# Performance work log

Measured on AMD Instinct MI355X. Metric: run time of the kernel, lower is better.

The kernel has to match this reference:

```python
import jax, jax.numpy as jnp
import numpy as np

N_BITS = 4096
CHANNELS = 48
WIDTH = 1024
HEIGHT = 1024


def setup_inputs() -> dict:
    key = jax.random.key(0)
    bits = jax.random.normal(key, (N_BITS,), dtype=jnp.float32)
    return {"bits": bits}


def reference(bits):
    # map_range = width*height // 8 * 8; with 1024x1024 this is exactly width*height
    map_range = (WIDTH * HEIGHT) // 8 * 8
    idx = jnp.arange(map_range) % N_BITS            # bit index for each pixel (row-major, x=i//W, y=i%W)
    vals = jnp.where(jnp.abs(bits[idx]) > 0.5, 1.0, 0.0).astype(jnp.float32)
    rows = map_range // WIDTH                        # == HEIGHT here (square map, fully covered)
    grid = jnp.zeros((WIDTH, HEIGHT), dtype=jnp.float32)
    grid = grid.at[:rows, :].set(vals.reshape(rows, WIDTH))
    # every channel gets an identical copy
    out = jnp.broadcast_to(grid[None, :, :], (CHANNELS, WIDTH, HEIGHT))
    return jnp.asarray(out)
```

## Files before the change

kernel.cpp:

```cpp
#include <hip/hip_runtime.h>


#define N4       12582912u
#define NBLK     2048u
#define NTHR     (NBLK * 256u)
#define NITER    (N4 / NTHR)

__global__ __launch_bounds__(256) void
LinearTextEmbedding_57604101374655_kernel(const float4* __restrict__ bits4,
                                          float4* __restrict__ out) {
    unsigned t = blockIdx.x * 256u + threadIdx.x;
    float4 b = bits4[t & 1023u];
    float4 v;
    v.x = (fabsf(b.x) > 0.5f) ? 1.0f : 0.0f;
    v.y = (fabsf(b.y) > 0.5f) ? 1.0f : 0.0f;
    v.z = (fabsf(b.z) > 0.5f) ? 1.0f : 0.0f;
    v.w = (fabsf(b.w) > 0.5f) ? 1.0f : 0.0f;
    float4* p = out + t;
#pragma unroll
    for (unsigned i = 0; i < NITER; ++i) {
        *p = v;
        p += NTHR;
    }
}

extern "C" void kernel_launch(void* const* d_in, const int* in_sizes, int n_in,
                              void* d_out, int out_size, void* d_ws, size_t ws_size,
                              hipStream_t stream) {
    const float4* bits4 = (const float4*)d_in[0];
    float4* out = (float4*)d_out;
    LinearTextEmbedding_57604101374655_kernel<<<NBLK, 256, 0, stream>>>(bits4, out);
}
```

Baseline: 195.8 us.

## Use many small blocks writing contiguous chunks with nontemporal stores

Replaces the persistent grid-stride loop (2048 blocks, 24 stores each) with 12288 blocks that each write one contiguous 16 KB chunk using four nontemporal vector stores. Each thread loads and binarizes four bit vectors. The aim is to cut cache pollution on the 201 MB write-only output and to improve write streaming. The cost is more block launches and redundant input loads per block.

```diff
diff --git a/kernel.cpp b/kernel.cpp
--- a/kernel.cpp
+++ b/kernel.cpp
@@ -1,33 +1,40 @@
 #include <hip/hip_runtime.h>
 
 
-#define N4       12582912u
-#define NBLK     2048u
-#define NTHR     (NBLK * 256u)
-#define NITER    (N4 / NTHR)
+typedef float v4f __attribute__((ext_vector_type(4)));
 
-__global__ __launch_bounds__(256) void
-LinearTextEmbedding_57604101374655_kernel(const float4* __restrict__ bits4,
-                                          float4* __restrict__ out) {
-    unsigned t = blockIdx.x * 256u + threadIdx.x;
-    float4 b = bits4[t & 1023u];
-    float4 v;
+#define N4    12582912u
+#define BLK4  1024u
+#define NBLK  (N4 / BLK4)
+
+__device__ __forceinline__ v4f bin4(v4f b) {
+    v4f v;
     v.x = (fabsf(b.x) > 0.5f) ? 1.0f : 0.0f;
     v.y = (fabsf(b.y) > 0.5f) ? 1.0f : 0.0f;
     v.z = (fabsf(b.z) > 0.5f) ? 1.0f : 0.0f;
     v.w = (fabsf(b.w) > 0.5f) ? 1.0f : 0.0f;
-    float4* p = out + t;
-#pragma unroll
-    for (unsigned i = 0; i < NITER; ++i) {
-        *p = v;
-        p += NTHR;
-    }
+    return v;
+}
+
+__global__ __launch_bounds__(256) void
+LinearTextEmbedding_57604101374655_kernel(const v4f* __restrict__ bits4,
+                                          v4f* __restrict__ out) {
+    unsigned tid  = threadIdx.x;
+    unsigned base = blockIdx.x * BLK4 + tid;
+    v4f v0 = bin4(bits4[tid]);
+    v4f v1 = bin4(bits4[256u + tid]);
+    v4f v2 = bin4(bits4[512u + tid]);
+    v4f v3 = bin4(bits4[768u + tid]);
+    __builtin_nontemporal_store(v0, &out[base]);
+    __builtin_nontemporal_store(v1, &out[base + 256u]);
+    __builtin_nontemporal_store(v2, &out[base + 512u]);
+    __builtin_nontemporal_store(v3, &out[base + 768u]);
 }
 
 extern "C" void kernel_launch(void* const* d_in, const int* in_sizes, int n_in,
                               void* d_out, int out_size, void* d_ws, size_t ws_size,
                               hipStream_t stream) {
-    const float4* bits4 = (const float4*)d_in[0];
-    float4* out = (float4*)d_out;
+    const v4f* bits4 = (const v4f*)d_in[0];
+    v4f* out = (v4f*)d_out;
     LinearTextEmbedding_57604101374655_kernel<<<NBLK, 256, 0, stream>>>(bits4, out);
 }
```

Measured after the change: 197.1 us, median of 2. About the same (+0.7%).
